# Kernel tuning notes

Hardware: AMD Instinct MI355X
Metric: run time of the kernel (lower is better)

## Reference

```python
import jax, jax.numpy as jnp
import numpy as np


def _expm_batch(S):
    # S: [..., m, m] skew-symmetric -> elementwise matrix exponential
    flat = S.reshape((-1,) + S.shape[-2:])
    E = jax.vmap(jax.scipy.linalg.expm)(flat)
    return E.reshape(S.shape)


def _time_prod(M):
    # M: [B, T, m, m] -> Z = M[:,T-1] @ ... @ M[:,0]  (dyadic, log-depth, matches DevNet dyadic_prod order)
    B, T, m, _ = M.shape
    eye = jnp.eye(m, dtype=M.dtype)
    while M.shape[1] > 1:
        if M.shape[1] % 2 == 1:
            pad = jnp.broadcast_to(eye, (B, 1, m, m))
            M = jnp.concatenate([M, pad], axis=1)
        # later factor on the left: M[:,1::2] @ M[:,0::2]
        M = jnp.einsum('btij,btjk->btik', M[:, 1::2], M[:, 0::2])
    return M[:, 0]


def setup_inputs() -> dict:
    key = jax.random.key(0)
    k1, k2, k3 = jax.random.split(key, 3)
    B, T, Cin, m, O = 64, 2048, 8, 16, 10
    X = jax.random.normal(k1, (B, T, Cin), dtype=jnp.float32)
    A = jax.random.normal(k2, (m, m, Cin), dtype=jnp.float32) * 0.2
    W = jax.random.normal(k3, (O, m * m), dtype=jnp.float32) * (1.0 / np.sqrt(m * m))
    b = jnp.zeros((O,), dtype=jnp.float32)
    return {"X": X, "A": A, "W": W, "b": b}


def reference(X, A, W, b):
    # skew-symmetric parametrization of the Lie algebra so(m)
    A_skew = A - jnp.swapaxes(A, 0, 1)          # [m, m, Cin]
    dX = X[:, 1:] - X[:, :-1]                    # [B, T-1, Cin] path increments
    S = jnp.einsum('btc,ijc->btij', dX, A_skew)  # [B, T-1, m, m] skew per step
    M = _expm_batch(S)                           # per-step SO(m) elements
    Z = _time_prod(M)                            # [B, m, m] path development
    out = Z.reshape(Z.shape[0], -1) @ W.T + b    # [B, n_outputs]
    return out
```

## Files before the change

### kernel.cpp

```cpp
#include <hip/hip_runtime.h>

#define BSZ   64
#define TLEN  2048
#define NSTEP 2047
#define CIN   8
#define NCH   128
#define CHL   16

typedef __attribute__((ext_vector_type(4))) float    fx4;
typedef __attribute__((ext_vector_type(4))) _Float16 hx4;

__device__ __forceinline__ hx4 pk4(float a, float b, float c, float d) {
    auto p0 = __builtin_amdgcn_cvt_pkrtz(a, b);
    auto p1 = __builtin_amdgcn_cvt_pkrtz(c, d);
    hx4 r; r[0] = p0[0]; r[1] = p0[1]; r[2] = p1[0]; r[3] = p1[1];
    return r;
}

__device__ __forceinline__ void splitf(const fx4 v, hx4& hi, hx4& lo) {
    _Float16 h0 = (_Float16)v[0], h1 = (_Float16)v[1];
    _Float16 h2 = (_Float16)v[2], h3 = (_Float16)v[3];
    hi[0] = h0; hi[1] = h1; hi[2] = h2; hi[3] = h3;
    lo = pk4(v[0] - (float)h0, v[1] - (float)h1, v[2] - (float)h2, v[3] - (float)h3);
}

__device__ __forceinline__ fx4 mm3(hx4 ah, hx4 al, hx4 bh, hx4 bl) {
    fx4 acc = {0.f, 0.f, 0.f, 0.f};
    acc = __builtin_amdgcn_mfma_f32_16x16x16f16(ah, bh, acc, 0, 0, 0);
    acc = __builtin_amdgcn_mfma_f32_16x16x16f16(ah, bl, acc, 0, 0, 0);
    acc = __builtin_amdgcn_mfma_f32_16x16x16f16(al, bh, acc, 0, 0, 0);
    return acc;
}

__device__ __forceinline__ void mfmaT(hx4 Mh, hx4 Ml, hx4 Ih, hx4& Th, hx4& Tl) {
    fx4 z = {0.f, 0.f, 0.f, 0.f};
    fx4 th = __builtin_amdgcn_mfma_f32_16x16x16f16(Mh, Ih, z, 0, 0, 0);
    fx4 tl = __builtin_amdgcn_mfma_f32_16x16x16f16(Ml, Ih, z, 0, 0, 0);
    Th = pk4(th[0], th[1], th[2], th[3]);
    Tl = pk4(tl[0], tl[1], tl[2], tl[3]);
}

__global__ __launch_bounds__(256)
void devnet_expm_chunk(const float* __restrict__ X, const float* __restrict__ A,
                       float* __restrict__ G)
{
    const int tid  = threadIdx.x;
    const int wid  = tid >> 6;
    const int lane = tid & 63;
    const int m    = lane >> 4;
    const int c    = lane & 15;
    const int gw   = blockIdx.x * 4 + wid;
    const int b    = gw >> 7;
    const int ch   = gw & (NCH - 1);

    float ask[4][CIN];
#pragma unroll
    for (int r = 0; r < 4; ++r) {
        const int i = 4 * m + r;
#pragma unroll
        for (int cc = 0; cc < CIN; ++cc)
            ask[r][cc] = A[(i * 16 + c) * CIN + cc] - A[(c * 16 + i) * CIN + cc];
    }

    fx4 idv;
#pragma unroll
    for (int r = 0; r < 4; ++r) idv[r] = (4 * m + r == c) ? 1.f : 0.f;
    const hx4 Ih = pk4(idv[0], idv[1], idv[2], idv[3]);

    fx4 P = idv;

    const int t0 = ch * CHL;
    const int t1 = (t0 + CHL < NSTEP) ? (t0 + CHL) : NSTEP;

    for (int t = t0; t < t1; ++t) {
        const float* xp = X + ((size_t)b * TLEN + t) * CIN;
        const float4 x0 = *reinterpret_cast<const float4*>(xp + 0);
        const float4 x1 = *reinterpret_cast<const float4*>(xp + 4);
        const float4 y0 = *reinterpret_cast<const float4*>(xp + 8);
        const float4 y1 = *reinterpret_cast<const float4*>(xp + 12);
        float dx[CIN];
        dx[0] = y0.x - x0.x; dx[1] = y0.y - x0.y; dx[2] = y0.z - x0.z; dx[3] = y0.w - x0.w;
        dx[4] = y1.x - x1.x; dx[5] = y1.y - x1.y; dx[6] = y1.z - x1.z; dx[7] = y1.w - x1.w;

        fx4 sv;
#pragma unroll
        for (int r = 0; r < 4; ++r) {
            float acc = 0.f;
#pragma unroll
            for (int cc = 0; cc < CIN; ++cc) acc = fmaf(dx[cc], ask[r][cc], acc);
            sv[r] = acc;
        }

        float a = fabsf(sv[0]) + fabsf(sv[1]) + fabsf(sv[2]) + fabsf(sv[3]);
        a += __shfl_xor(a, 16, 64);
        a += __shfl_xor(a, 32, 64);
        a = fmaxf(a, __shfl_xor(a, 1, 64));
        a = fmaxf(a, __shfl_xor(a, 2, 64));
        a = fmaxf(a, __shfl_xor(a, 4, 64));
        a = fmaxf(a, __shfl_xor(a, 8, 64));

        int e;
        (void)frexpf(a, &e);
        int sc = e + 2;
        if (sc < 0) sc = 0;
        const float scale = ldexpf(1.0f, -sc);

        fx4 xv = sv * scale;
        fx4 nxv = -xv;
        hx4 Xah, Xal;
        splitf(nxv, Xah, Xal);

        fx4 R;
#pragma unroll
        for (int r = 0; r < 4; ++r) R[r] = fmaf(xv[r], 0.2f, idv[r]);
#pragma unroll
        for (int k = 4; k >= 1; --k) {
            hx4 Rh, Rl;
            splitf(R, Rh, Rl);
            fx4 acc = mm3(Xah, Xal, Rh, Rl);
            const float inv = 1.f / (float)k;
#pragma unroll
            for (int r = 0; r < 4; ++r) R[r] = fmaf(acc[r], inv, idv[r]);
        }

        for (int q = 0; q < sc; ++q) {
            hx4 Rh, Rl, Th, Tl;
            splitf(R, Rh, Rl);
            mfmaT(Rh, Rl, Ih, Th, Tl);
            R = mm3(Th, Tl, Rh, Rl);
        }

        {
            hx4 Rh, Rl, Th, Tl, Ph, Pl;
            splitf(R, Rh, Rl);
            mfmaT(Rh, Rl, Ih, Th, Tl);
            splitf(P, Ph, Pl);
            P = mm3(Th, Tl, Ph, Pl);
        }
    }

    *reinterpret_cast<fx4*>(G + ((size_t)b * NCH + ch) * 256 + lane * 4) = P;
}

__global__ __launch_bounds__(256)
void devnet_reduce1(float* __restrict__ G)
{
    const int tid  = threadIdx.x;
    const int wid  = tid >> 6;
    const int lane = tid & 63;
    const int m    = lane >> 4;
    const int c    = lane & 15;
    const int gw   = blockIdx.x * 4 + wid;
    const int b    = gw >> 4;
    const int w    = gw & 15;

    fx4 idv;
#pragma unroll
    for (int r = 0; r < 4; ++r) idv[r] = (4 * m + r == c) ? 1.f : 0.f;
    const hx4 Ih = pk4(idv[0], idv[1], idv[2], idv[3]);

    float* base = G + ((size_t)b * NCH + w * 8) * 256;

    fx4 Acc = *reinterpret_cast<const fx4*>(base + lane * 4);
    for (int cc = 1; cc < 8; ++cc) {
        fx4 Q = *reinterpret_cast<const fx4*>(base + (size_t)cc * 256 + lane * 4);
        hx4 Qh, Ql, Th, Tl, Bh, Bl;
        splitf(Q, Qh, Ql);
        mfmaT(Qh, Ql, Ih, Th, Tl);
        splitf(Acc, Bh, Bl);
        Acc = mm3(Th, Tl, Bh, Bl);
    }
    *reinterpret_cast<fx4*>(base + lane * 4) = Acc;
}

__global__ __launch_bounds__(64)
void devnet_reduce2(const float* __restrict__ G, const float* __restrict__ W,
                    const float* __restrict__ bias, float* __restrict__ out)
{
    __shared__ float Zf[256];

    const int lane = threadIdx.x;
    const int m    = lane >> 4;
    const int c    = lane & 15;
    const int b    = blockIdx.x;

    fx4 idv;
#pragma unroll
    for (int r = 0; r < 4; ++r) idv[r] = (4 * m + r == c) ? 1.f : 0.f;
    const hx4 Ih = pk4(idv[0], idv[1], idv[2], idv[3]);

    const float* gb = G + (size_t)b * NCH * 256;

    fx4 Acc = *reinterpret_cast<const fx4*>(gb + lane * 4);
    for (int k = 1; k < 16; ++k) {
        fx4 Q = *reinterpret_cast<const fx4*>(gb + (size_t)(k * 8) * 256 + lane * 4);
        hx4 Qh, Ql, Th, Tl, Bh, Bl;
        splitf(Q, Qh, Ql);
        mfmaT(Qh, Ql, Ih, Th, Tl);
        splitf(Acc, Bh, Bl);
        Acc = mm3(Th, Tl, Bh, Bl);
    }

#pragma unroll
    for (int r = 0; r < 4; ++r) Zf[(4 * m + r) * 16 + c] = Acc[r];

    for (int o = 0; o < 10; ++o) {
        const float* wo = W + o * 256;
        float v = Zf[lane] * wo[lane];
        v = fmaf(Zf[lane + 64],  wo[lane + 64],  v);
        v = fmaf(Zf[lane + 128], wo[lane + 128], v);
        v = fmaf(Zf[lane + 192], wo[lane + 192], v);
#pragma unroll
        for (int off = 32; off >= 1; off >>= 1) v += __shfl_down(v, off, 64);
        if (lane == 0) out[b * 10 + o] = v + bias[o];
    }
}

extern "C" void kernel_launch(void* const* d_in, const int* in_sizes, int n_in,
                              void* d_out, int out_size, void* d_ws, size_t ws_size,
                              hipStream_t stream)
{
    const float* X    = (const float*)d_in[0];
    const float* A    = (const float*)d_in[1];
    const float* W    = (const float*)d_in[2];
    const float* bias = (const float*)d_in[3];
    float* out = (float*)d_out;
    float* G   = (float*)d_ws;

    devnet_expm_chunk<<<BSZ * NCH / 4, 256, 0, stream>>>(X, A, G);
    devnet_reduce1<<<BSZ * 16 / 4, 256, 0, stream>>>(G);
    devnet_reduce2<<<BSZ, 64, 0, stream>>>(G, W, bias, out);
}
```

Measured before the change: 195.4 us.

## Process two time chunks per wave for ILP and merge reduction kernels

Result: faster. 180.8 us (-7.5%).

```diff
diff --git a/kernel.cpp b/kernel.cpp
--- a/kernel.cpp
+++ b/kernel.cpp
@@ -40,7 +40,42 @@
     Tl = pk4(tl[0], tl[1], tl[2], tl[3]);
 }
 
-__global__ __launch_bounds__(256)
+__device__ __forceinline__ fx4 foldQ(fx4 Q, fx4 Acc, hx4 Ih) {
+    hx4 Qh, Ql, Th, Tl, Bh, Bl;
+    splitf(Q, Qh, Ql);
+    mfmaT(Qh, Ql, Ih, Th, Tl);
+    splitf(Acc, Bh, Bl);
+    return mm3(Th, Tl, Bh, Bl);
+}
+
+__device__ __forceinline__ float infnorm(fx4 sv) {
+    float a = fabsf(sv[0]) + fabsf(sv[1]) + fabsf(sv[2]) + fabsf(sv[3]);
+    a += __shfl_xor(a, 16, 64);
+    a += __shfl_xor(a, 32, 64);
+    a = fmaxf(a, __shfl_xor(a, 1, 64));
+    a = fmaxf(a, __shfl_xor(a, 2, 64));
+    a = fmaxf(a, __shfl_xor(a, 4, 64));
+    a = fmaxf(a, __shfl_xor(a, 8, 64));
+    return a;
+}
+
+__device__ __forceinline__ void loadDx(const float* __restrict__ X, int b, int t,
+                                       float dx[CIN]) {
+    if (t < NSTEP) {
+        const float* xp = X + ((size_t)b * TLEN + t) * CIN;
+        const float4 x0 = *reinterpret_cast<const float4*>(xp + 0);
+        const float4 x1 = *reinterpret_cast<const float4*>(xp + 4);
+        const float4 y0 = *reinterpret_cast<const float4*>(xp + 8);
+        const float4 y1 = *reinterpret_cast<const float4*>(xp + 12);
+        dx[0] = y0.x - x0.x; dx[1] = y0.y - x0.y; dx[2] = y0.z - x0.z; dx[3] = y0.w - x0.w;
+        dx[4] = y1.x - x1.x; dx[5] = y1.y - x1.y; dx[6] = y1.z - x1.z; dx[7] = y1.w - x1.w;
+    } else {
+#pragma unroll
+        for (int i = 0; i < CIN; ++i) dx[i] = 0.f;
+    }
+}
+
+__global__ __launch_bounds__(256, 4)
 void devnet_expm_chunk(const float* __restrict__ X, const float* __restrict__ A,
                        float* __restrict__ G)
 {
@@ -50,8 +85,8 @@
     const int m    = lane >> 4;
     const int c    = lane & 15;
     const int gw   = blockIdx.x * 4 + wid;
-    const int b    = gw >> 7;
-    const int ch   = gw & (NCH - 1);
+    const int b    = gw >> 6;
+    const int ch0  = gw & 63;
 
     float ask[4][CIN];
 #pragma unroll
@@ -67,152 +102,139 @@
     for (int r = 0; r < 4; ++r) idv[r] = (4 * m + r == c) ? 1.f : 0.f;
     const hx4 Ih = pk4(idv[0], idv[1], idv[2], idv[3]);
 
-    fx4 P = idv;
-
-    const int t0 = ch * CHL;
-    const int t1 = (t0 + CHL < NSTEP) ? (t0 + CHL) : NSTEP;
-
-    for (int t = t0; t < t1; ++t) {
-        const float* xp = X + ((size_t)b * TLEN + t) * CIN;
-        const float4 x0 = *reinterpret_cast<const float4*>(xp + 0);
-        const float4 x1 = *reinterpret_cast<const float4*>(xp + 4);
-        const float4 y0 = *reinterpret_cast<const float4*>(xp + 8);
-        const float4 y1 = *reinterpret_cast<const float4*>(xp + 12);
-        float dx[CIN];
-        dx[0] = y0.x - x0.x; dx[1] = y0.y - x0.y; dx[2] = y0.z - x0.z; dx[3] = y0.w - x0.w;
-        dx[4] = y1.x - x1.x; dx[5] = y1.y - x1.y; dx[6] = y1.z - x1.z; dx[7] = y1.w - x1.w;
-
-        fx4 sv;
+    fx4 P0 = idv, P1 = idv;
+
+    for (int tt = 0; tt < CHL; ++tt) {
+        const int ta = ch0 * CHL + tt;
+        const int tb = (ch0 + 64) * CHL + tt;
+
+        float dxa[CIN], dxb[CIN];
+        loadDx(X, b, ta, dxa);
+        loadDx(X, b, tb, dxb);
+
+        fx4 sa, sb;
 #pragma unroll
         for (int r = 0; r < 4; ++r) {
-            float acc = 0.f;
-#pragma unroll
-            for (int cc = 0; cc < CIN; ++cc) acc = fmaf(dx[cc], ask[r][cc], acc);
-            sv[r] = acc;
-        }
-
-        float a = fabsf(sv[0]) + fabsf(sv[1]) + fabsf(sv[2]) + fabsf(sv[3]);
-        a += __shfl_xor(a, 16, 64);
-        a += __shfl_xor(a, 32, 64);
-        a = fmaxf(a, __shfl_xor(a, 1, 64));
-        a = fmaxf(a, __shfl_xor(a, 2, 64));
-        a = fmaxf(a, __shfl_xor(a, 4, 64));
-        a = fmaxf(a, __shfl_xor(a, 8, 64));
-
-        int e;
-        (void)frexpf(a, &e);
-        int sc = e + 2;
+            float va = 0.f, vb = 0.f;
+#pragma unroll
+            for (int cc = 0; cc < CIN; ++cc) {
+                va = fmaf(dxa[cc], ask[r][cc], va);
+                vb = fmaf(dxb[cc], ask[r][cc], vb);
+            }
+            sa[r] = va; sb[r] = vb;
+        }
+
+        const float na = infnorm(sa);
+        const float nb = infnorm(sb);
+        int ea, eb;
+        (void)frexpf(na, &ea);
+        (void)frexpf(nb, &eb);
+        int sc = (ea > eb ? ea : eb) + 2;
         if (sc < 0) sc = 0;
         const float scale = ldexpf(1.0f, -sc);
 
-        fx4 xv = sv * scale;
-        fx4 nxv = -xv;
-        hx4 Xah, Xal;
-        splitf(nxv, Xah, Xal);
-
-        fx4 R;
-#pragma unroll
-        for (int r = 0; r < 4; ++r) R[r] = fmaf(xv[r], 0.2f, idv[r]);
+        fx4 xa = sa * scale, xb = sb * scale;
+        hx4 XahA, XalA, XahB, XalB;
+        {
+            fx4 nxa = -xa, nxb = -xb;
+            splitf(nxa, XahA, XalA);
+            splitf(nxb, XahB, XalB);
+        }
+
+        fx4 Ra, Rb;
+#pragma unroll
+        for (int r = 0; r < 4; ++r) {
+            Ra[r] = fmaf(xa[r], 0.2f, idv[r]);
+            Rb[r] = fmaf(xb[r], 0.2f, idv[r]);
+        }
 #pragma unroll
         for (int k = 4; k >= 1; --k) {
-            hx4 Rh, Rl;
-            splitf(R, Rh, Rl);
-            fx4 acc = mm3(Xah, Xal, Rh, Rl);
+            hx4 RhA, RlA, RhB, RlB;
+            splitf(Ra, RhA, RlA);
+            splitf(Rb, RhB, RlB);
+            fx4 qa = mm3(XahA, XalA, RhA, RlA);
+            fx4 qb = mm3(XahB, XalB, RhB, RlB);
             const float inv = 1.f / (float)k;
 #pragma unroll
-            for (int r = 0; r < 4; ++r) R[r] = fmaf(acc[r], inv, idv[r]);
+            for (int r = 0; r < 4; ++r) {
+                Ra[r] = fmaf(qa[r], inv, idv[r]);
+                Rb[r] = fmaf(qb[r], inv, idv[r]);
+            }
         }
 
         for (int q = 0; q < sc; ++q) {
-            hx4 Rh, Rl, Th, Tl;
-            splitf(R, Rh, Rl);
-            mfmaT(Rh, Rl, Ih, Th, Tl);
-            R = mm3(Th, Tl, Rh, Rl);
-        }
-
-        {
-            hx4 Rh, Rl, Th, Tl, Ph, Pl;
-            splitf(R, Rh, Rl);
-            mfmaT(Rh, Rl, Ih, Th, Tl);
-            splitf(P, Ph, Pl);
-            P = mm3(Th, Tl, Ph, Pl);
-        }
-    }
-
-    *reinterpret_cast<fx4*>(G + ((size_t)b * NCH + ch) * 256 + lane * 4) = P;
+            hx4 RhA, RlA, ThA, TlA, RhB, RlB, ThB, TlB;
+            splitf(Ra, RhA, RlA);
+            splitf(Rb, RhB, RlB);
+            mfmaT(RhA, RlA, Ih, ThA, TlA);
+            mfmaT(RhB, RlB, Ih, ThB, TlB);
+            Ra = mm3(ThA, TlA, RhA, RlA);
+            Rb = mm3(ThB, TlB, RhB, RlB);
+        }
+
+        P0 = foldQ(Ra, P0, Ih);
+        P1 = foldQ(Rb, P1, Ih);
+    }
+
+    float* gp = G + ((size_t)b * NCH) * 256;
+    *reinterpret_cast<fx4*>(gp + (size_t)ch0 * 256 + lane * 4)        = P0;
+    *reinterpret_cast<fx4*>(gp + (size_t)(ch0 + 64) * 256 + lane * 4) = P1;
 }
 
 __global__ __launch_bounds__(256)
-void devnet_reduce1(float* __restrict__ G)
+void devnet_reduce(const float* __restrict__ G, const float* __restrict__ W,
+                   const float* __restrict__ bias, float* __restrict__ out)
 {
+    __shared__ __align__(16) float Fs[4][256];
+    __shared__ float Zf[256];
+
     const int tid  = threadIdx.x;
     const int wid  = tid >> 6;
     const int lane = tid & 63;
     const int m    = lane >> 4;
     const int c    = lane & 15;
-    const int gw   = blockIdx.x * 4 + wid;
-    const int b    = gw >> 4;
-    const int w    = gw & 15;
+    const int b    = blockIdx.x;
 
     fx4 idv;
 #pragma unroll
     for (int r = 0; r < 4; ++r) idv[r] = (4 * m + r == c) ? 1.f : 0.f;
     const hx4 Ih = pk4(idv[0], idv[1], idv[2], idv[3]);
 
-    float* base = G + ((size_t)b * NCH + w * 8) * 256;
-
-    fx4 Acc = *reinterpret_cast<const fx4*>(base + lane * 4);
-    for (int cc = 1; cc < 8; ++cc) {
-        fx4 Q = *reinterpret_cast<const fx4*>(base + (size_t)cc * 256 + lane * 4);
-        hx4 Qh, Ql, Th, Tl, Bh, Bl;
-        splitf(Q, Qh, Ql);
-        mfmaT(Qh, Ql, Ih, Th, Tl);
-        splitf(Acc, Bh, Bl);
-        Acc = mm3(Th, Tl, Bh, Bl);
-    }
-    *reinterpret_cast<fx4*>(base + lane * 4) = Acc;
-}
-
-__global__ __launch_bounds__(64)
-void devnet_reduce2(const float* __restrict__ G, const float* __restrict__ W,
-                    const float* __restrict__ bias, float* __restrict__ out)
-{
-    __shared__ float Zf[256];
-
-    const int lane = threadIdx.x;
-    const int m    = lane >> 4;
-    const int c    = lane & 15;
-    const int b    = blockIdx.x;
-
-    fx4 idv;
-#pragma unroll
-    for (int r = 0; r < 4; ++r) idv[r] = (4 * m + r == c) ? 1.f : 0.f;
-    const hx4 Ih = pk4(idv[0], idv[1], idv[2], idv[3]);
-
-    const float* gb = G + (size_t)b * NCH * 256;
-
-    fx4 Acc = *reinterpret_cast<const fx4*>(gb + lane * 4);
+    const float* gb    = G + (size_t)b * NCH * 256;
+    const float* baseA = gb + (size_t)(wid * 32) * 256;
+    const float* baseB = gb + (size_t)(wid * 32 + 16) * 256;
+
+    fx4 AccA = *reinterpret_cast<const fx4*>(baseA + lane * 4);
+    fx4 AccB = *reinterpret_cast<const fx4*>(baseB + lane * 4);
     for (int k = 1; k < 16; ++k) {
-        fx4 Q = *reinterpret_cast<const fx4*>(gb + (size_t)(k * 8) * 256 + lane * 4);
-        hx4 Qh, Ql, Th, Tl, Bh, Bl;
-        splitf(Q, Qh, Ql);
-        mfmaT(Qh, Ql, Ih, Th, Tl);
-        splitf(Acc, Bh, Bl);
-        Acc = mm3(Th, Tl, Bh, Bl);
-    }
-
-#pragma unroll
-    for (int r = 0; r < 4; ++r) Zf[(4 * m + r) * 16 + c] = Acc[r];
-
-    for (int o = 0; o < 10; ++o) {
-        const float* wo = W + o * 256;
-        float v = Zf[lane] * wo[lane];
-        v = fmaf(Zf[lane + 64],  wo[lane + 64],  v);
-        v = fmaf(Zf[lane + 128], wo[lane + 128], v);
-        v = fmaf(Zf[lane + 192], wo[lane + 192], v);
-#pragma unroll
-        for (int off = 32; off >= 1; off >>= 1) v += __shfl_down(v, off, 64);
-        if (lane == 0) out[b * 10 + o] = v + bias[o];
+        fx4 Qa = *reinterpret_cast<const fx4*>(baseA + (size_t)k * 256 + lane * 4);
+        fx4 Qb = *reinterpret_cast<const fx4*>(baseB + (size_t)k * 256 + lane * 4);
+        AccA = foldQ(Qa, AccA, Ih);
+        AccB = foldQ(Qb, AccB, Ih);
+    }
+    fx4 Acc = foldQ(AccB, AccA, Ih);
+    *reinterpret_cast<fx4*>(&Fs[wid][lane * 4]) = Acc;
+    __syncthreads();
+
+    if (wid == 0) {
+        fx4 Z = *reinterpret_cast<const fx4*>(&Fs[0][lane * 4]);
+        for (int w = 1; w < 4; ++w) {
+            fx4 Q = *reinterpret_cast<const fx4*>(&Fs[w][lane * 4]);
+            Z = foldQ(Q, Z, Ih);
+        }
+#pragma unroll
+        for (int r = 0; r < 4; ++r) Zf[(4 * m + r) * 16 + c] = Z[r];
+
+        for (int o = 0; o < 10; ++o) {
+            const float* wo = W + o * 256;
+            float v = Zf[lane] * wo[lane];
+            v = fmaf(Zf[lane + 64],  wo[lane + 64],  v);
+            v = fmaf(Zf[lane + 128], wo[lane + 128], v);
+            v = fmaf(Zf[lane + 192], wo[lane + 192], v);
+#pragma unroll
+            for (int off = 32; off >= 1; off >>= 1) v += __shfl_down(v, off, 64);
+            if (lane == 0) out[b * 10 + o] = v + bias[o];
+        }
     }
 }
 
@@ -227,7 +249,6 @@
     float* out = (float*)d_out;
     float* G   = (float*)d_ws;
 
-    devnet_expm_chunk<<<BSZ * NCH / 4, 256, 0, stream>>>(X, A, G);
-    devnet_reduce1<<<BSZ * 16 / 4, 256, 0, stream>>>(G);
-    devnet_reduce2<<<BSZ, 64, 0, stream>>>(G, W, bias, out);
-}
+    devnet_expm_chunk<<<BSZ * NCH / 8, 256, 0, stream>>>(X, A, G);
+    devnet_reduce<<<BSZ, 256, 0, stream>>>(G, W, bias, out);
+}
```
